# Kernel optimization log

Measured on AMD Instinct MI355X. Metric: run time of the kernel, lower is better.

The kernel has to match this reference:

```python
import jax, jax.numpy as jnp
import numpy as np

N = 100000
E1 = 600000
E2 = 300000
H = 128
IN = 35
G = 1000
EPS = 1e-5


def _rbf(d):
    # d: [E] distances -> [E, 9] gaussian RBF on [0, 6] with 9 centers
    mu = jnp.linspace(0.0, 6.0, 9, dtype=d.dtype)
    sigma = 6.0 / 9.0
    return jnp.exp(-(((d[:, None] - mu) / sigma) ** 2))


def _bn_eval(x, g, b):
    # BatchNorm1d in eval mode with running_mean=0, running_var=1
    return g * x * (1.0 / np.sqrt(1.0 + EPS)) + b


def _leaky(x):
    return jnp.where(x >= 0, x, 0.01 * x)


def _branch(h, pos, edge_index, cW, cB, nW, nB, g, b):
    row, col = edge_index[0], edge_index[1]
    d = jnp.linalg.norm(pos[row] - pos[col], axis=-1)          # [E]
    radial = jax.nn.silu(_rbf(d) @ cW + cB)                    # [E, H]
    msg = h[row] * radial                                      # gather-mul
    agg = jax.ops.segment_sum(msg, col, num_segments=h.shape[0])  # scatter-add
    return _bn_eval(_leaky((h + agg) @ nW + nB), g, b)


def setup_inputs() -> dict:
    key = jax.random.key(0)
    ks = jax.random.split(key, 16)
    s = lambda fan: 1.0 / np.sqrt(fan)
    inp = {
        "x": jax.random.normal(ks[0], (N, IN), jnp.float32),
        "pos": jax.random.normal(ks[1], (N, 3), jnp.float32) * 2.0,
        "W_in": jax.random.normal(ks[2], (IN, H), jnp.float32) * s(IN),
        "b_in": jnp.zeros((H,), jnp.float32),
        "coordW": jax.random.normal(ks[3], (3, 2, 9, H), jnp.float32) * s(9),
        "coordB": jnp.zeros((3, 2, H), jnp.float32),
        "nodeW": jax.random.normal(ks[4], (3, 2, H, H), jnp.float32) * s(H),
        "nodeB": jnp.zeros((3, 2, H), jnp.float32),
        "bnG": jnp.ones((3, 2, H), jnp.float32),
        "bnB": jnp.zeros((3, 2, H), jnp.float32),
        "fcW": jax.random.normal(ks[5], (3, H, H), jnp.float32) * s(H),
        "fcB": jnp.zeros((3, H), jnp.float32),
        "fcBnG": jnp.ones((3, H), jnp.float32),
        "fcBnB": jnp.zeros((3, H), jnp.float32),
        "outW": jax.random.normal(ks[6], (H, 1), jnp.float32) * s(H),
        "outB": jnp.zeros((1,), jnp.float32),
        "edge_index_intra": jax.random.randint(ks[7], (2, E1), 0, N, jnp.int32),
        "edge_index_inter": jax.random.randint(ks[8], (2, E2), 0, N, jnp.int32),
        "batch": jnp.sort(jax.random.randint(ks[9], (N,), 0, G, jnp.int32)),
    }
    return inp


def reference(x, pos, W_in, b_in, coordW, coordB, nodeW, nodeB, bnG, bnB,
              fcW, fcB, fcBnG, fcBnB, outW, outB,
              edge_index_intra, edge_index_inter, batch):
    h = jax.nn.silu(x @ W_in + b_in)
    for l in range(3):  # 3 GraphInteractionLayers
        intra = _branch(h, pos, edge_index_intra, coordW[l, 0], coordB[l, 0],
                        nodeW[l, 0], nodeB[l, 0], bnG[l, 0], bnB[l, 0])
        inter = _branch(h, pos, edge_index_inter, coordW[l, 1], coordB[l, 1],
                        nodeW[l, 1], nodeB[l, 1], bnG[l, 1], bnB[l, 1])
        h = intra + inter
    hg = jax.ops.segment_sum(h, batch, num_segments=G)  # global_add_pool [G, H]
    for i in range(3):
        hg = _bn_eval(_leaky(hg @ fcW[i] + fcB[i]), fcBnG[i], fcBnB[i])
    out = hg @ outW + outB  # [G, 1]
    return out.reshape(-1)
```

## Files before the change

### kernel.cpp

```cpp
#include <hip/hip_runtime.h>
#include <hip/hip_fp16.h>
#include <math.h>

#define NN   100000
#define HH   128
#define INF_ 35
#define GG   1000
#define GBM  128
#define NBINS 2048
#define DSCALE 128.0f
#define DINV   0.0078125f
#define DCLAMP 15.992f

typedef __attribute__((ext_vector_type(8))) short short8;
typedef __attribute__((ext_vector_type(4))) float f32x4;

static __device__ __forceinline__ float silu_f(float x){ return x / (1.f + __expf(-x)); }
static __device__ __forceinline__ unsigned bf16rne(float x){
    unsigned u = __float_as_uint(x);
    return (u + 0x7FFFu + ((u>>16)&1u)) >> 16;
}
#define BN_INV 0.9999950000374997f

__global__ void k_count(const int* __restrict__ ei1, const int* __restrict__ ei2,
                        int E1, int E2, int n, int* __restrict__ deg){
    int e = blockIdx.x*256 + threadIdx.x;
    int ET = E1 + E2;
    if (e >= ET) return;
    int c;
    if (e < E1) c = ei1[E1 + e];
    else        c = n + ei2[E2 + (e - E1)];
    atomicAdd(&deg[c], 1);
}

__global__ void k_scan_lb(const int* __restrict__ deg, int n2, int* __restrict__ off,
                          int* __restrict__ agg, int* __restrict__ incl,
                          unsigned* __restrict__ flags, int ET){
    __shared__ int s[256];
    __shared__ int exc_sh;
    int blk = blockIdx.x, tid = threadIdx.x;
    int i = blk*256 + tid;
    int v = (i<n2)? deg[i] : 0;
    s[tid] = v; __syncthreads();
    for (int ofs=1; ofs<256; ofs<<=1){
        int t = (tid>=ofs)? s[tid-ofs] : 0;
        __syncthreads(); s[tid] += t; __syncthreads();
    }
    if (tid == 0){
        int total = s[255];
        atomicExch(&agg[blk], total);
        __threadfence();
        atomicExch(&flags[blk], 1u);
        int exc = 0;
        int pb = blk - 1;
        while (pb >= 0){
            unsigned f;
            do { f = atomicAdd(&flags[pb], 0u); } while (f == 0u);
            if (f == 2u){ exc += atomicAdd(&incl[pb], 0); break; }
            exc += atomicAdd(&agg[pb], 0);
            pb--;
        }
        atomicExch(&incl[blk], exc + total);
        __threadfence();
        atomicExch(&flags[blk], 2u);
        exc_sh = exc;
    }
    __syncthreads();
    if (i < n2) off[i] = exc_sh + s[tid] - v;
    if (i == 0) off[n2] = ET;
}

__global__ void k_build(const float* __restrict__ nodeW,
                        const float* __restrict__ coordW, const float* __restrict__ coordB,
                        const float* __restrict__ W_in,
                        const int* __restrict__ ei1, const int* __restrict__ ei2,
                        int E1, int E2, int n, const float* __restrict__ pos,
                        const int* __restrict__ off, int* __restrict__ cur,
                        unsigned short* __restrict__ Bpk, unsigned short* __restrict__ tabs,
                        float* __restrict__ Wtg, float2* __restrict__ rec){
    int blk = blockIdx.x, tx = threadIdx.x;
    if (blk < 48){
        int idx = blk*256 + tx;
        if (idx >= 6*2048) return;
        int li = idx >> 11;
        int r  = idx & 2047;
        int s  = r >> 9;
        int r2 = r & 511;
        int ct = r2 >> 6;
        int l  = r2 & 63;
        const float* src = nodeW + (size_t)li*16384 + (size_t)(s*32 + (l>>4)*8)*HH + ct*16 + (l&15);
        unsigned short o[8];
        #pragma unroll
        for (int j=0;j<8;j++) o[j] = (unsigned short)bf16rne(src[(size_t)j*HH]);
        uint4 v;
        v.x = o[0] | ((unsigned)o[1]<<16);
        v.y = o[2] | ((unsigned)o[3]<<16);
        v.z = o[4] | ((unsigned)o[5]<<16);
        v.w = o[6] | ((unsigned)o[7]<<16);
        *(uint4*)(Bpk + (size_t)idx*8) = v;
    } else if (blk < 66){
        int i = (blk-48)*256 + tx;
        if (i >= 128*36) return;
        int c = i/36, k = i - c*36;
        Wtg[i] = (k < INF_) ? W_in[k*HH + c] : 0.f;
    } else if (blk < 66+6144){
        int idx = (blk-66)*256 + tx;
        if (idx >= 6*NBINS*HH) return;
        int li  = idx / (NBINS*HH);
        int rem = idx - li*(NBINS*HH);
        int bin = rem >> 7;
        int col = rem & 127;
        float d0 = (float)bin * DINV;
        float d1 = d0 + DINV;
        const float* cW = coordW + (size_t)li*9*HH;
        float cb = coordB[li*HH + col];
        float q0 = cb, q1 = cb;
        #pragma unroll
        for (int k=0;k<9;k++){
            float wk = cW[k*HH + col];
            float t0 = 1.5f*d0 - 1.125f*(float)k;
            float t1 = 1.5f*d1 - 1.125f*(float)k;
            q0 += __expf(-t0*t0) * wk;
            q1 += __expf(-t1*t1) * wk;
        }
        float v = silu_f(q0);
        float s = silu_f(q1) - v;
        tabs[(size_t)idx*2+0] = __half_as_ushort(__float2half_rn(v));
        tabs[(size_t)idx*2+1] = __half_as_ushort(__float2half_rn(s));
    } else {
        int e = (blk - (66+6144))*256 + tx;
        int ET = E1 + E2;
        if (e >= ET) return;
        int r, creal, cslot;
        if (e < E1){ r = ei1[e];        creal = ei1[E1 + e];        cslot = creal; }
        else       { int ee = e - E1; r = ei2[ee]; creal = ei2[E2 + ee]; cslot = n + creal; }
        int slot = atomicAdd(&cur[cslot], 1);
        int p = off[cslot] + slot;
        float dx = pos[r*3+0]-pos[creal*3+0];
        float dy = pos[r*3+1]-pos[creal*3+1];
        float dz = pos[r*3+2]-pos[creal*3+2];
        float d  = sqrtf(dx*dx + dy*dy + dz*dz);
        rec[p] = make_float2(__int_as_float(r), d);
    }
}

#define NT_IN (NN/16)
__global__ __launch_bounds__(256) void k_input(const float* __restrict__ x,
        const float* __restrict__ Wtg, const float* __restrict__ b,
        unsigned short* __restrict__ hb){
    __shared__ __align__(16) float xs[16][36];
    int tx = threadIdx.x;
    int c = tx & 127, g = tx >> 7;
    float bc = b[c];
    const float4* wp = (const float4*)(Wtg + c*36);
    for (int tile = blockIdx.x; tile < NT_IN; tile += gridDim.x){
        int r0 = tile*16;
        for (int i = tx; i < 16*INF_; i += 256){
            int rr = i/INF_, kk = i - rr*INF_;
            xs[rr][kk] = x[(size_t)(r0+rr)*INF_ + kk];
        }
        if (tx < 16) xs[tx][35] = 0.f;
        __syncthreads();
        float acc[8];
        #pragma unroll
        for (int j=0;j<8;j++) acc[j] = bc;
        #pragma unroll
        for (int kk=0;kk<9;kk++){
            float4 w4 = wp[kk];
            #pragma unroll
            for (int j=0;j<8;j++){
                float4 xv = *(const float4*)(&xs[g*8+j][kk*4]);
                acc[j] += xv.x*w4.x + xv.y*w4.y + xv.z*w4.z + xv.w*w4.w;
            }
        }
        #pragma unroll
        for (int j=0;j<8;j++){
            int gr = r0 + g*8 + j;
            hb[(size_t)gr*HH + c] = (unsigned short)bf16rne(silu_f(acc[j]));
        }
        __syncthreads();
    }
}

#define GEDGE(RP, S_, B_, F_)                                        \
    int S_ = __float_as_int((RP).x);                                 \
    float db_##S_ = fminf((RP).y, DCLAMP)*DSCALE;                    \
    int B_ = (int)db_##S_; float F_ = db_##S_ - (float)B_;

#define GACC(U_, T_, F_)                                             \
    {                                                                \
        float2 p0 = __half22float2(*(const __half2*)&(T_).x);        \
        float2 p1 = __half22float2(*(const __half2*)&(T_).y);        \
        acc.x += __uint_as_float((U_)<<16)           * (p0.x + p0.y*(F_)); \
        acc.y += __uint_as_float((U_) & 0xFFFF0000u) * (p1.x + p1.y*(F_)); \
    }

__global__ __launch_bounds__(256) void k_gather(
        const unsigned short* __restrict__ hb,
        const int* __restrict__ off, const float2* __restrict__ rec,
        const unsigned short* __restrict__ tab0, const unsigned short* __restrict__ tab1,
        unsigned short* __restrict__ aggb1, unsigned short* __restrict__ aggb2,
        int n, int nblk1){
    int b = blockIdx.x;
    int br = (b >= nblk1) ? 1 : 0;
    int node = (br ? b - nblk1 : b)*4 + (threadIdx.x>>6);
    if (node >= n) return;
    int c = (threadIdx.x & 63)*2;
    const unsigned short* tab = br ? tab1 : tab0;
    unsigned short* aggp = br ? aggb2 : aggb1;

    float2 acc;
    {
        unsigned u = *(const unsigned*)(hb + (size_t)node*HH + c);
        acc.x = __uint_as_float(u<<16); acc.y = __uint_as_float(u & 0xFFFF0000u);
    }

    int slot = node + br*n;
    int lo = off[slot], hi = off[slot+1];
    lo = __builtin_amdgcn_readfirstlane(lo);
    hi = __builtin_amdgcn_readfirstlane(hi);

    int p = lo;
    for (; p+4<=hi; p+=4){
        float2 r0 = rec[p], r1 = rec[p+1], r2 = rec[p+2], r3 = rec[p+3];
        GEDGE(r0, s0, b0, f0)
        GEDGE(r1, s1, b1, f1)
        GEDGE(r2, s2, b2, f2)
        GEDGE(r3, s3, b3, f3)
        unsigned u0 = *(const unsigned*)(hb + (size_t)s0*HH + c);
        unsigned u1 = *(const unsigned*)(hb + (size_t)s1*HH + c);
        unsigned u2 = *(const unsigned*)(hb + (size_t)s2*HH + c);
        unsigned u3 = *(const unsigned*)(hb + (size_t)s3*HH + c);
        uint2 t0 = *(const uint2*)(tab + ((size_t)b0*HH + c)*2);
        uint2 t1 = *(const uint2*)(tab + ((size_t)b1*HH + c)*2);
        uint2 t2 = *(const uint2*)(tab + ((size_t)b2*HH + c)*2);
        uint2 t3 = *(const uint2*)(tab + ((size_t)b3*HH + c)*2);
        GACC(u0, t0, f0)
        GACC(u1, t1, f1)
        GACC(u2, t2, f2)
        GACC(u3, t3, f3)
    }
    for (; p+2<=hi; p+=2){
        float2 r0 = rec[p], r1 = rec[p+1];
        GEDGE(r0, s0, b0, f0)
        GEDGE(r1, s1, b1, f1)
        unsigned u0 = *(const unsigned*)(hb + (size_t)s0*HH + c);
        unsigned u1 = *(const unsigned*)(hb + (size_t)s1*HH + c);
        uint2 t0 = *(const uint2*)(tab + ((size_t)b0*HH + c)*2);
        uint2 t1 = *(const uint2*)(tab + ((size_t)b1*HH + c)*2);
        GACC(u0, t0, f0)
        GACC(u1, t1, f1)
    }
    if (p < hi){
        float2 r0 = rec[p];
        GEDGE(r0, s0, b0, f0)
        unsigned u0 = *(const unsigned*)(hb + (size_t)s0*HH + c);
        uint2 t0 = *(const uint2*)(tab + ((size_t)b0*HH + c)*2);
        GACC(u0, t0, f0)
    }
    unsigned pk = bf16rne(acc.x) | (bf16rne(acc.y)<<16);
    *(unsigned*)(aggp + (size_t)node*HH + c) = pk;
}

__global__ __launch_bounds__(256) void k_gemm2m(
        const unsigned short* __restrict__ A1, const unsigned short* __restrict__ A2,
        const unsigned short* __restrict__ Bp0, const unsigned short* __restrict__ Bp1,
        const float* __restrict__ b1, const float* __restrict__ b2,
        const float* __restrict__ g1, const float* __restrict__ g2,
        const float* __restrict__ e1, const float* __restrict__ e2,
        float* __restrict__ C, unsigned short* __restrict__ Cb, int n){
    int tx = threadIdx.x;
    int l = tx & 63, wv = tx >> 6;
    int rb = blockIdx.x*GBM + wv*32;
    int mlo = l & 15, khi = l >> 4;
    int ar0 = rb + mlo, ar1 = rb + 16 + mlo;
    bool ok0 = ar0 < n, ok1 = ar1 < n;

    f32x4 accA[2][8], accB[2][8];
    #pragma unroll
    for (int rh=0;rh<2;rh++)
        #pragma unroll
        for (int ct=0;ct<8;ct++){ accA[rh][ct] = (f32x4)0.f; accB[rh][ct] = (f32x4)0.f; }

    {
        short8 af0[4], af1[4];
        const short8* ap0 = (const short8*)(A1 + (size_t)ar0*HH);
        const short8* ap1 = (const short8*)(A1 + (size_t)ar1*HH);
        #pragma unroll
        for (int s=0;s<4;s++){
            af0[s] = ok0 ? ap0[s*4 + khi] : (short8)0;
            af1[s] = ok1 ? ap1[s*4 + khi] : (short8)0;
        }
        const short8* bp = (const short8*)Bp0;
        #pragma unroll
        for (int s=0;s<4;s++){
            #pragma unroll
            for (int ct=0;ct<8;ct++){
                short8 bf = bp[s*512 + ct*64 + l];
                accA[0][ct] = __builtin_amdgcn_mfma_f32_16x16x32_bf16(af0[s], bf, accA[0][ct], 0, 0, 0);
                accA[1][ct] = __builtin_amdgcn_mfma_f32_16x16x32_bf16(af1[s], bf, accA[1][ct], 0, 0, 0);
            }
        }
    }
    {
        short8 af0[4], af1[4];
        const short8* ap0 = (const short8*)(A2 + (size_t)ar0*HH);
        const short8* ap1 = (const short8*)(A2 + (size_t)ar1*HH);
        #pragma unroll
        for (int s=0;s<4;s++){
            af0[s] = ok0 ? ap0[s*4 + khi] : (short8)0;
            af1[s] = ok1 ? ap1[s*4 + khi] : (short8)0;
        }
        const short8* bp = (const short8*)Bp1;
        #pragma unroll
        for (int s=0;s<4;s++){
            #pragma unroll
            for (int ct=0;ct<8;ct++){
                short8 bf = bp[s*512 + ct*64 + l];
                accB[0][ct] = __builtin_amdgcn_mfma_f32_16x16x32_bf16(af0[s], bf, accB[0][ct], 0, 0, 0);
                accB[1][ct] = __builtin_amdgcn_mfma_f32_16x16x32_bf16(af1[s], bf, accB[1][ct], 0, 0, 0);
            }
        }
    }

    #pragma unroll
    for (int ct=0;ct<8;ct++){
        int ncol = ct*16 + mlo;
        float bi1 = b1[ncol], ga1 = g1[ncol], bt1 = e1[ncol];
        float bi2 = b2[ncol], ga2 = g2[ncol], bt2 = e2[ncol];
        #pragma unroll
        for (int rh=0;rh<2;rh++){
            #pragma unroll
            for (int r=0;r<4;r++){
                int grow = rb + rh*16 + khi*4 + r;
                if (grow < n){
                    float xv = accA[rh][ct][r] + bi1;
                    xv = (xv>=0.f)? xv : 0.01f*xv;
                    float yv = accB[rh][ct][r] + bi2;
                    yv = (yv>=0.f)? yv : 0.01f*yv;
                    float o = (ga1*xv + ga2*yv)*BN_INV + bt1 + bt2;
                    if (C) C[(size_t)grow*HH + ncol] = o;
                    Cb[(size_t)grow*HH + ncol] = (unsigned short)bf16rne(o);
                }
            }
        }
    }
}

static __device__ __forceinline__ int lower_bound_i(const int* __restrict__ a, int n, int key){
    int lo=0, hi=n;
    while (lo<hi){ int m=(lo+hi)>>1; if (a[m]<key) lo=m+1; else hi=m; }
    return lo;
}
__global__ void k_poolfc(const float* __restrict__ h,
                     const int* __restrict__ batch,
                     const float* __restrict__ fcW, const float* __restrict__ fcB,
                     const float* __restrict__ fbg, const float* __restrict__ fbb,
                     const float* __restrict__ outW, const float* __restrict__ outB,
                     float* __restrict__ out, int n){
    __shared__ float row[HH];
    __shared__ float red[2];
    int g = blockIdx.x, c = threadIdx.x;
    int lo = lower_bound_i(batch, n, g);
    int hi = lower_bound_i(batch, n, g+1);
    float v = 0.f;
    for (int r=lo; r<hi; r++) v += h[(size_t)r*HH + c];
    for (int l=0;l<3;l++){
        row[c] = v; __syncthreads();
        float acc = fcB[l*HH + c];
        const float* W = fcW + (size_t)l*HH*HH;
        #pragma unroll 8
        for (int k=0;k<HH;k++) acc += row[k]*W[k*HH + c];
        acc = (acc>=0.f)? acc : 0.01f*acc;
        v = fbg[l*HH+c]*acc*BN_INV + fbb[l*HH+c];
        __syncthreads();
    }
    float t = v * outW[c];
    #pragma unroll
    for (int o=32;o>0;o>>=1) t += __shfl_down(t, o, 64);
    if ((c&63)==0) red[c>>6] = t;
    __syncthreads();
    if (c==0) out[g] = red[0] + red[1] + outB[0];
}

extern "C" void kernel_launch(void* const* d_in, const int* in_sizes, int n_in,
                              void* d_out, int out_size, void* d_ws, size_t ws_size,
                              hipStream_t stream){
    const float* x      = (const float*)d_in[0];
    const float* pos    = (const float*)d_in[1];
    const float* W_in   = (const float*)d_in[2];
    const float* b_in   = (const float*)d_in[3];
    const float* coordW = (const float*)d_in[4];
    const float* coordB = (const float*)d_in[5];
    const float* nodeW  = (const float*)d_in[6];
    const float* nodeB  = (const float*)d_in[7];
    const float* bnG    = (const float*)d_in[8];
    const float* bnB    = (const float*)d_in[9];
    const float* fcW    = (const float*)d_in[10];
    const float* fcB    = (const float*)d_in[11];
    const float* fcBnG  = (const float*)d_in[12];
    const float* fcBnB  = (const float*)d_in[13];
    const float* outW   = (const float*)d_in[14];
    const float* outB   = (const float*)d_in[15];
    const int* ei1      = (const int*)d_in[16];
    const int* ei2      = (const int*)d_in[17];
    const int* batch    = (const int*)d_in[18];
    const int E1 = in_sizes[16]/2, E2 = in_sizes[17]/2;
    const int n = NN;
    const int n2 = 2*n;
    const int ET = E1 + E2;

    char* w = (char*)d_ws;
    size_t o = 0;
    auto alloc = [&](size_t bytes)->void*{
        void* r = w + o;
        o += (bytes + 255) & ~(size_t)255;
        return r;
    };
    unsigned short* hb    = (unsigned short*)alloc((size_t)n*HH*2);
    unsigned short* hb2   = (unsigned short*)alloc((size_t)n*HH*2);
    unsigned short* aggb1 = (unsigned short*)alloc((size_t)n*HH*2);
    unsigned short* aggb2 = (unsigned short*)alloc((size_t)n*HH*2);
    unsigned short* Bpk   = (unsigned short*)alloc((size_t)6*16384*2);
    unsigned short* tabs  = (unsigned short*)alloc((size_t)6*NBINS*HH*4);
    float*  Wtg  = (float*)alloc((size_t)128*36*4);
    int*    off  = (int*)alloc((size_t)(n2+1)*4);
    int*    cnt  = (int*)alloc((size_t)n2*4);
    int*    cur  = (int*)alloc((size_t)n2*4);
    unsigned* flags = (unsigned*)alloc(1024*4);
    int*    aggl = (int*)alloc(1024*4);
    int*    incl = (int*)alloc(1024*4);
    float2* rec  = (float2*)alloc((size_t)ET*8);
    float*  hfin = (float*)alloc((size_t)n*HH*4);
    (void)n_in; (void)out_size; (void)ws_size;

    int nb2 = (n2+255)/256;

    hipMemsetAsync(cnt, 0, (size_t)(2*n2 + 1024)*4, stream);
    k_count<<<(ET+255)/256,256,0,stream>>>(ei1, ei2, E1, E2, n, cnt);
    k_scan_lb<<<nb2,256,0,stream>>>(cnt, n2, off, aggl, incl, flags, ET);
    k_build<<<66+6144+(ET+255)/256,256,0,stream>>>(nodeW, coordW, coordB, W_in,
        ei1, ei2, E1, E2, n, pos, off, cur, Bpk, tabs, Wtg, rec);

    k_input<<<2048,256,0,stream>>>(x, Wtg, b_in, hb);

    int nb4 = (n+3)/4;
    unsigned short* hbcur = hb;
    unsigned short* hboth = hb2;
    for (int l=0; l<3; l++){
        int li0 = l*2, li1 = l*2+1;
        float* Cout = (l==2) ? hfin : nullptr;
        k_gather<<<2*nb4,256,0,stream>>>(hbcur, off, rec,
            tabs + (size_t)li0*NBINS*HH*2, tabs + (size_t)li1*NBINS*HH*2,
            aggb1, aggb2, n, nb4);
        k_gemm2m<<<(n+GBM-1)/GBM,256,0,stream>>>(aggb1, aggb2,
            Bpk + (size_t)li0*16384, Bpk + (size_t)li1*16384,
            nodeB + (size_t)li0*HH,  nodeB + (size_t)li1*HH,
            bnG   + (size_t)li0*HH,  bnG   + (size_t)li1*HH,
            bnB   + (size_t)li0*HH,  bnB   + (size_t)li1*HH,
            Cout, hboth, n);
        unsigned short* tb = hbcur; hbcur = hboth; hboth = tb;
    }

    k_poolfc<<<GG,128,0,stream>>>(hfin, batch, fcW, fcB, fcBnG, fcBnB, outW, outB, (float*)d_out, n);
}
```

Measured before the change: 620.4 us.

## Shrink GEMM block to 16 rows per wave with per-column-tile accumulators

The node GEMM kernel now processes 16 rows per wave (64 per block) instead of 32, and computes each 16-column output tile's two accumulators just before its epilogue instead of holding all 32 accumulator vectors live. This cuts accumulator register pressure to raise occupancy and doubles the grid size. In exchange, the B weight fragments are loaded once per 16 rows rather than once per 32, doubling weight traffic per output row, and MFMA chains per tile are short and dependent.

```diff
diff --git a/kernel.cpp b/kernel.cpp
--- a/kernel.cpp
+++ b/kernel.cpp
@@ -6,7 +6,7 @@
 #define HH   128
 #define INF_ 35
 #define GG   1000
-#define GBM  128
+#define LBM  64
 #define NBINS 2048
 #define DSCALE 128.0f
 #define DINV   0.0078125f
@@ -271,77 +271,48 @@
         float* __restrict__ C, unsigned short* __restrict__ Cb, int n){
     int tx = threadIdx.x;
     int l = tx & 63, wv = tx >> 6;
-    int rb = blockIdx.x*GBM + wv*32;
+    int rb = blockIdx.x*LBM + wv*16;
     int mlo = l & 15, khi = l >> 4;
-    int ar0 = rb + mlo, ar1 = rb + 16 + mlo;
-    bool ok0 = ar0 < n, ok1 = ar1 < n;
-
-    f32x4 accA[2][8], accB[2][8];
-    #pragma unroll
-    for (int rh=0;rh<2;rh++)
-        #pragma unroll
-        for (int ct=0;ct<8;ct++){ accA[rh][ct] = (f32x4)0.f; accB[rh][ct] = (f32x4)0.f; }
-
+    int arow = rb + mlo;
+    bool ok = arow < n;
+
+    short8 af0[4], af1[4];
     {
-        short8 af0[4], af1[4];
-        const short8* ap0 = (const short8*)(A1 + (size_t)ar0*HH);
-        const short8* ap1 = (const short8*)(A1 + (size_t)ar1*HH);
+        const short8* ap0 = (const short8*)(A1 + (size_t)arow*HH);
+        const short8* ap1 = (const short8*)(A2 + (size_t)arow*HH);
         #pragma unroll
         for (int s=0;s<4;s++){
-            af0[s] = ok0 ? ap0[s*4 + khi] : (short8)0;
-            af1[s] = ok1 ? ap1[s*4 + khi] : (short8)0;
-        }
-        const short8* bp = (const short8*)Bp0;
-        #pragma unroll
-        for (int s=0;s<4;s++){
-            #pragma unroll
-            for (int ct=0;ct<8;ct++){
-                short8 bf = bp[s*512 + ct*64 + l];
-                accA[0][ct] = __builtin_amdgcn_mfma_f32_16x16x32_bf16(af0[s], bf, accA[0][ct], 0, 0, 0);
-                accA[1][ct] = __builtin_amdgcn_mfma_f32_16x16x32_bf16(af1[s], bf, accA[1][ct], 0, 0, 0);
-            }
-        }
-    }
-    {
-        short8 af0[4], af1[4];
-        const short8* ap0 = (const short8*)(A2 + (size_t)ar0*HH);
-        const short8* ap1 = (const short8*)(A2 + (size_t)ar1*HH);
-        #pragma unroll
-        for (int s=0;s<4;s++){
-            af0[s] = ok0 ? ap0[s*4 + khi] : (short8)0;
-            af1[s] = ok1 ? ap1[s*4 + khi] : (short8)0;
-        }
-        const short8* bp = (const short8*)Bp1;
-        #pragma unroll
-        for (int s=0;s<4;s++){
-            #pragma unroll
-            for (int ct=0;ct<8;ct++){
-                short8 bf = bp[s*512 + ct*64 + l];
-                accB[0][ct] = __builtin_amdgcn_mfma_f32_16x16x32_bf16(af0[s], bf, accB[0][ct], 0, 0, 0);
-                accB[1][ct] = __builtin_amdgcn_mfma_f32_16x16x32_bf16(af1[s], bf, accB[1][ct], 0, 0, 0);
-            }
-        }
-    }
+            af0[s] = ok ? ap0[s*4 + khi] : (short8)0;
+            af1[s] = ok ? ap1[s*4 + khi] : (short8)0;
+        }
+    }
+    const short8* bp0 = (const short8*)Bp0;
+    const short8* bp1 = (const short8*)Bp1;
 
     #pragma unroll
     for (int ct=0;ct<8;ct++){
+        f32x4 a0 = (f32x4)0.f, a1 = (f32x4)0.f;
+        #pragma unroll
+        for (int s=0;s<4;s++)
+            a0 = __builtin_amdgcn_mfma_f32_16x16x32_bf16(af0[s], bp0[s*512 + ct*64 + l], a0, 0, 0, 0);
+        #pragma unroll
+        for (int s=0;s<4;s++)
+            a1 = __builtin_amdgcn_mfma_f32_16x16x32_bf16(af1[s], bp1[s*512 + ct*64 + l], a1, 0, 0, 0);
+
         int ncol = ct*16 + mlo;
         float bi1 = b1[ncol], ga1 = g1[ncol], bt1 = e1[ncol];
         float bi2 = b2[ncol], ga2 = g2[ncol], bt2 = e2[ncol];
         #pragma unroll
-        for (int rh=0;rh<2;rh++){
-            #pragma unroll
-            for (int r=0;r<4;r++){
-                int grow = rb + rh*16 + khi*4 + r;
-                if (grow < n){
-                    float xv = accA[rh][ct][r] + bi1;
-                    xv = (xv>=0.f)? xv : 0.01f*xv;
-                    float yv = accB[rh][ct][r] + bi2;
-                    yv = (yv>=0.f)? yv : 0.01f*yv;
-                    float o = (ga1*xv + ga2*yv)*BN_INV + bt1 + bt2;
-                    if (C) C[(size_t)grow*HH + ncol] = o;
-                    Cb[(size_t)grow*HH + ncol] = (unsigned short)bf16rne(o);
-                }
+        for (int r=0;r<4;r++){
+            int grow = rb + khi*4 + r;
+            if (grow < n){
+                float xv = a0[r] + bi1;
+                xv = (xv>=0.f)? xv : 0.01f*xv;
+                float yv = a1[r] + bi2;
+                yv = (yv>=0.f)? yv : 0.01f*yv;
+                float o = (ga1*xv + ga2*yv)*BN_INV + bt1 + bt2;
+                if (C) C[(size_t)grow*HH + ncol] = o;
+                Cb[(size_t)grow*HH + ncol] = (unsigned short)bf16rne(o);
             }
         }
     }
@@ -453,7 +424,7 @@
         k_gather<<<2*nb4,256,0,stream>>>(hbcur, off, rec,
             tabs + (size_t)li0*NBINS*HH*2, tabs + (size_t)li1*NBINS*HH*2,
             aggb1, aggb2, n, nb4);
-        k_gemm2m<<<(n+GBM-1)/GBM,256,0,stream>>>(aggb1, aggb2,
+        k_gemm2m<<<(n+LBM-1)/LBM,256,0,stream>>>(aggb1, aggb2,
             Bpk + (size_t)li0*16384, Bpk + (size_t)li1*16384,
             nodeB + (size_t)li0*HH,  nodeB + (size_t)li1*HH,
             bnG   + (size_t)li0*HH,  bnG   + (size_t)li1*HH,
```

After: 506.3 us. -18.4%, faster.
